# Performance work log

Hardware: AMD Instinct MI355X
Metric: run time of the kernel (lower is better)

Reference implementation:

```python
import jax, jax.numpy as jnp
import numpy as np

N, C, E = 50000, 64, 800000
EPS = 1e-5

def _ln(h, g, b):
    mu = jnp.mean(h, axis=-1, keepdims=True)
    var = jnp.var(h, axis=-1, keepdims=True)
    return (h - mu) * jax.lax.rsqrt(var + EPS) * g + b

def setup_inputs() -> dict:
    key = jax.random.key(0)
    ks = jax.random.split(key, 16)
    def w(k, i, o):
        return jax.random.normal(k, (i, o), jnp.float32) * (1.0 / np.sqrt(i))
    return {
        "x": jax.random.normal(ks[0], (N, C), jnp.float32),
        "edge_index": jax.random.randint(ks[1], (2, E), 0, N, jnp.int32),
        # structure_predictor: Linear(2C,256) -> LN(256) -> GELU -> Dropout(eval) -> Linear(256,1)
        "sp_w1": w(ks[2], 2 * C, 256), "sp_b1": jnp.zeros((256,), jnp.float32),
        "sp_g": jnp.ones((256,), jnp.float32), "sp_be": jnp.zeros((256,), jnp.float32),
        "sp_w2": w(ks[3], 256, 1), "sp_b2": jnp.zeros((1,), jnp.float32),
        # feature_reconstructor: Linear(C,2C) -> LN(2C) -> GELU -> Dropout(eval) -> Linear(2C,C)
        "fr_w1": w(ks[4], C, 2 * C), "fr_b1": jnp.zeros((2 * C,), jnp.float32),
        "fr_g": jnp.ones((2 * C,), jnp.float32), "fr_be": jnp.zeros((2 * C,), jnp.float32),
        "fr_w2": w(ks[5], 2 * C, C), "fr_b2": jnp.zeros((C,), jnp.float32),
        # projection_head: Linear(C,256) -> LN(256) -> GELU -> Linear(256,128)
        "ph_w1": w(ks[6], C, 256), "ph_b1": jnp.zeros((256,), jnp.float32),
        "ph_g": jnp.ones((256,), jnp.float32), "ph_be": jnp.zeros((256,), jnp.float32),
        "ph_w2": w(ks[7], 256, 128), "ph_b2": jnp.zeros((128,), jnp.float32),
    }

def reference(x, edge_index, sp_w1, sp_b1, sp_g, sp_be, sp_w2, sp_b2,
              fr_w1, fr_b1, fr_g, fr_be, fr_w2, fr_b2,
              ph_w1, ph_b1, ph_g, ph_be, ph_w2, ph_b2):
    row, col = edge_index[0], edge_index[1]
    edge_features = jnp.concatenate([x[row], x[col]], axis=1)  # [E, 2C]
    h = _ln(edge_features @ sp_w1 + sp_b1, sp_g, sp_be)
    structure_pred = jax.nn.gelu(h, approximate=False) @ sp_w2 + sp_b2  # [E, 1]
    h = _ln(x @ fr_w1 + fr_b1, fr_g, fr_be)
    reconstructed = jax.nn.gelu(h, approximate=False) @ fr_w2 + fr_b2  # [N, C]
    h = _ln(x @ ph_w1 + ph_b1, ph_g, ph_be)
    projected = jax.nn.gelu(h, approximate=False) @ ph_w2 + ph_b2  # [N, 128]
    return (structure_pred, reconstructed, projected)
```

## Files before the change

### kernel.cpp

```cpp
#include <hip/hip_runtime.h>
#include <hip/hip_bf16.h>

typedef __attribute__((ext_vector_type(8))) short short8;
typedef __attribute__((ext_vector_type(4))) float f32x4;

#define MFMA(a, b, c) __builtin_amdgcn_mfma_f32_16x16x32_bf16((a), (b), (c), 0, 0, 0)

__device__ __forceinline__ unsigned short f2bf(float f) {
    unsigned int u = __float_as_uint(f);
    u += 0x7fffu + ((u >> 16) & 1u);
    return (unsigned short)(u >> 16);
}

__device__ __forceinline__ unsigned int cvt_pk_bf16(float lo, float hi) {
    unsigned int d;
    asm("v_cvt_pk_bf16_f32 %0, %1, %2" : "=v"(d) : "v"(lo), "v"(hi));
    return d;
}

template<int CTRL>
__device__ __forceinline__ float dpp_addf(float v) {
    int t = __builtin_amdgcn_update_dpp(0, __float_as_int(v), CTRL, 0xF, 0xF, true);
    return v + __int_as_float(t);
}
__device__ __forceinline__ float rowsum16(float v) {
    v = dpp_addf<0x121>(v);
    v = dpp_addf<0x122>(v);
    v = dpp_addf<0x124>(v);
    v = dpp_addf<0x128>(v);
    return v;
}

#if __has_builtin(__builtin_amdgcn_exp2f)
#define EXP2(x) __builtin_amdgcn_exp2f(x)
#else
#define EXP2(x) __expf((x) * 0.69314718f)
#endif

__device__ __forceinline__ float gelu_fast(float x) {
    float a = x * __builtin_fmaf(x * x, 0.10295427f, 2.3021210f);
    float E = EXP2(a);
    float r = __builtin_amdgcn_rcpf(E + 1.0f);
    return __builtin_fmaf(-x, r, x);
}

__device__ __forceinline__ short8 load_bfrag(const float* __restrict__ w, int k0, int n, int ldn) {
    short8 r;
#pragma unroll
    for (int u = 0; u < 8; ++u)
        r[u] = (short)f2bf(w[(k0 + u) * ldn + n]);
    return r;
}

template<int N1P>
struct SmemMlp {
    unsigned short sS[64 * N1P];
    float rstat[64 * 8];
};

template<int K, int N1, int N2, int MI>
__device__ void mlp_tile(SmemMlp<N1 + 8>& sm, const float* __restrict__ x,
                         const float* __restrict__ w1, const float* __restrict__ b1,
                         const float* __restrict__ g, const float* __restrict__ be,
                         const float* __restrict__ w2, const float* __restrict__ b2,
                         float* __restrict__ out, int Nrows, int t) {
    constexpr int R = MI * 16;
    constexpr int KP = K + 8, N1P = N1 + 8;
    constexpr int CPW1 = N1 / 4;
    constexpr int JT1 = CPW1 / 16;
    constexpr int KK1 = K / 32;
    constexpr int KK2 = N1 / 32;
    constexpr int JT2 = N2 / 64;
    constexpr int TPR = 256 / R;
    constexpr int FPT = K / TPR;
    constexpr int F4 = FPT / 4;

    const int tid = threadIdx.x;
    const int wave = tid >> 6, lane = tid & 63;
    const int l15 = lane & 15, quad = lane >> 4;
    const int r0 = t * R;

    {
        int m0 = tid / TPR, pp = tid % TPR;
        int rowg = r0 + m0; if (rowg >= Nrows) rowg = Nrows - 1;
        const float4* src = (const float4*)(x + (long)rowg * K + pp * FPT);
        unsigned short* dst = &sm.sS[m0 * KP + pp * FPT];
#pragma unroll
        for (int u = 0; u < F4; ++u) {
            float4 f = src[u];
            ushort4 h; h.x = f2bf(f.x); h.y = f2bf(f.y); h.z = f2bf(f.z); h.w = f2bf(f.w);
            *(ushort4*)(dst + 4 * u) = h;
        }
    }

    short8 breg1[JT1][KK1];
#pragma unroll
    for (int j = 0; j < JT1; ++j)
#pragma unroll
        for (int kk = 0; kk < KK1; ++kk)
            breg1[j][kk] = load_bfrag(w1, kk * 32 + quad * 8, CPW1 * wave + 16 * j + l15, N1);

    float b1v[JT1], gv[JT1], bev[JT1];
#pragma unroll
    for (int j = 0; j < JT1; ++j) {
        int c = CPW1 * wave + 16 * j + l15;
        b1v[j] = b1[c]; gv[j] = g[c]; bev[j] = be[c];
    }
    float b2v[JT2];
#pragma unroll
    for (int j = 0; j < JT2; ++j) b2v[j] = b2[wave * 16 * JT2 + 16 * j + l15];

    __syncthreads();

    f32x4 acc1[MI][JT1];
#pragma unroll
    for (int i = 0; i < MI; ++i)
#pragma unroll
        for (int j = 0; j < JT1; ++j)
            acc1[i][j] = (f32x4){0.f, 0.f, 0.f, 0.f};

#pragma unroll
    for (int kk = 0; kk < KK1; ++kk) {
        short8 a[MI];
#pragma unroll
        for (int i = 0; i < MI; ++i)
            a[i] = *(const short8*)&sm.sS[(16 * i + l15) * KP + kk * 32 + quad * 8];
#pragma unroll
        for (int i = 0; i < MI; ++i)
#pragma unroll
            for (int j = 0; j < JT1; ++j)
                acc1[i][j] = MFMA(a[i], breg1[j][kk], acc1[i][j]);
    }

#pragma unroll
    for (int i = 0; i < MI; ++i)
#pragma unroll
        for (int r = 0; r < 4; ++r) {
            float s = 0.f, ss = 0.f;
#pragma unroll
            for (int j = 0; j < JT1; ++j) {
                float v = acc1[i][j][r] + b1v[j];
                acc1[i][j][r] = v;
                s += v; ss = __builtin_fmaf(v, v, ss);
            }
            s = rowsum16(s); ss = rowsum16(ss);
            if (l15 == 0) {
                int row = 16 * i + quad * 4 + r;
                *(float2*)&sm.rstat[row * 8 + wave * 2] = make_float2(s, ss);
            }
        }
    __syncthreads();

#pragma unroll
    for (int i = 0; i < MI; ++i)
#pragma unroll
        for (int r = 0; r < 4; ++r) {
            int row = 16 * i + quad * 4 + r;
            const float4* st = (const float4*)&sm.rstat[row * 8];
            float4 q0 = st[0], q1 = st[1];
            float s  = (q0.x + q0.z) + (q1.x + q1.z);
            float ss = (q0.y + q0.w) + (q1.y + q1.w);
            float mean = s * (1.f / (float)N1);
            float var  = __builtin_fmaf(ss, 1.f / (float)N1, -mean * mean);
            float rstd = __builtin_amdgcn_rsqf(var + 1e-5f);
            float nm = -mean * rstd;
#pragma unroll
            for (int j = 0; j < JT1; ++j) {
                float tt = __builtin_fmaf(acc1[i][j][r], rstd, nm);
                float xn = __builtin_fmaf(tt, gv[j], bev[j]);
                sm.sS[row * N1P + CPW1 * wave + 16 * j + l15] = f2bf(gelu_fast(xn));
            }
        }
    __syncthreads();

    f32x4 acc2[MI][JT2];
#pragma unroll
    for (int i = 0; i < MI; ++i)
#pragma unroll
        for (int j = 0; j < JT2; ++j)
            acc2[i][j] = (f32x4){0.f, 0.f, 0.f, 0.f};

#pragma unroll
    for (int kk = 0; kk < KK2; ++kk) {
        short8 bf[JT2];
#pragma unroll
        for (int j = 0; j < JT2; ++j)
            bf[j] = load_bfrag(w2, kk * 32 + quad * 8, wave * 16 * JT2 + 16 * j + l15, N2);
        short8 a[MI];
#pragma unroll
        for (int i = 0; i < MI; ++i)
            a[i] = *(const short8*)&sm.sS[(16 * i + l15) * N1P + kk * 32 + quad * 8];
#pragma unroll
        for (int i = 0; i < MI; ++i)
#pragma unroll
            for (int j = 0; j < JT2; ++j)
                acc2[i][j] = MFMA(a[i], bf[j], acc2[i][j]);
    }

#pragma unroll
    for (int i = 0; i < MI; ++i)
#pragma unroll
        for (int r = 0; r < 4; ++r) {
            int rowg = r0 + 16 * i + quad * 4 + r;
            if (rowg < Nrows) {
#pragma unroll
                for (int j = 0; j < JT2; ++j)
                    out[(long)rowg * N2 + wave * 16 * JT2 + 16 * j + l15] = acc2[i][j][r] + b2v[j];
            }
        }
}

__device__ void proj_tile(unsigned short* sX , const float* __restrict__ x,
                          const float* __restrict__ w1, const float* __restrict__ b1,
                          unsigned short* __restrict__ P, int N, int tile, int isB) {
    constexpr int KP = 72;
    const int tid = threadIdx.x;
    const int wave = tid >> 6, lane = tid & 63;
    const int l15 = lane & 15, quad = lane >> 4;
    const int r0 = tile * 64;

    {
        int m0 = tid >> 2, pp = tid & 3;
        int rowg = r0 + m0; if (rowg >= N) rowg = N - 1;
        const float4* src = (const float4*)(x + (long)rowg * 64 + pp * 16);
        unsigned short* dst = &sX[m0 * KP + pp * 16];
#pragma unroll
        for (int u = 0; u < 4; ++u) {
            float4 f = src[u];
            ushort4 h; h.x = f2bf(f.x); h.y = f2bf(f.y); h.z = f2bf(f.z); h.w = f2bf(f.w);
            *(ushort4*)(dst + 4 * u) = h;
        }
    }

    short8 breg[4][2];
#pragma unroll
    for (int j = 0; j < 4; ++j)
#pragma unroll
        for (int kk = 0; kk < 2; ++kk)
            breg[j][kk] = load_bfrag(w1, isB * 64 + kk * 32 + quad * 8, wave * 64 + 16 * j + l15, 256);

    float b1v[4];
#pragma unroll
    for (int j = 0; j < 4; ++j)
        b1v[j] = isB ? 0.f : b1[wave * 64 + 16 * j + l15];

    __syncthreads();

    f32x4 acc[4][4];
#pragma unroll
    for (int i = 0; i < 4; ++i)
#pragma unroll
        for (int j = 0; j < 4; ++j)
            acc[i][j] = (f32x4){0.f, 0.f, 0.f, 0.f};

#pragma unroll
    for (int kk = 0; kk < 2; ++kk) {
        short8 a[4];
#pragma unroll
        for (int i = 0; i < 4; ++i)
            a[i] = *(const short8*)&sX[(16 * i + l15) * KP + kk * 32 + quad * 8];
#pragma unroll
        for (int i = 0; i < 4; ++i)
#pragma unroll
            for (int j = 0; j < 4; ++j)
                acc[i][j] = MFMA(a[i], breg[j][kk], acc[i][j]);
    }

#pragma unroll
    for (int i = 0; i < 4; ++i)
#pragma unroll
        for (int r = 0; r < 4; ++r) {
            int rowg = r0 + 16 * i + quad * 4 + r;
            if (rowg < N) {
                uint2 d;
                d.x = cvt_pk_bf16(acc[i][0][r] + b1v[0], acc[i][1][r] + b1v[1]);
                d.y = cvt_pk_bf16(acc[i][2][r] + b1v[2], acc[i][3][r] + b1v[3]);
                *(uint2*)(P + (long)rowg * 256 + wave * 64 + l15 * 4) = d;
            }
        }
}

__device__ __forceinline__ int clamp_e(long v, int E) {
    return v < (long)E ? (int)v : E - 1;
}

__device__ void edge_role2(const unsigned short* __restrict__ Pa,
                           const unsigned short* __restrict__ Pb,
                           const int* __restrict__ ei,
                           const float* __restrict__ g, const float* __restrict__ be,
                           const float* __restrict__ w2, const float* __restrict__ b2,
                           float* __restrict__ out, int E, int ebid, int nebk) {
    const int tid = threadIdx.x;
    const int lane = tid & 63;
    const int quad = lane >> 4, l15 = lane & 15;

    float gv[16], bev[16], w2v[16];
#pragma unroll
    for (int u = 0; u < 16; ++u) {
        int c = ((l15 >> 2) << 6) + ((u & 3) << 4) + ((l15 & 3) << 2) + (u >> 2);
        gv[u] = g[c]; bev[u] = be[c]; w2v[u] = w2[c];
    }
    const float b2v = b2[0];

    const int wid = ebid * 4 + (tid >> 6);
    const long stride = (long)nebk * 16L;
    long base = (long)wid * 4;
    if (base >= E) return;

    int ir1, ic1;
    uint4 cA0, cA1, cB0, cB1;
    {
        int e0 = clamp_e(base + quad, E);
        int r = ei[e0], c = ei[E + e0];
        const uint4* pa = (const uint4*)(Pa + (long)r * 256 + l15 * 16);
        const uint4* pb = (const uint4*)(Pb + (long)c * 256 + l15 * 16);
        cA0 = pa[0]; cA1 = pa[1]; cB0 = pb[0]; cB1 = pb[1];
        int e1 = clamp_e(base + stride + quad, E);
        ir1 = ei[e1]; ic1 = ei[E + e1];
    }

    for (; base < E; base += stride) {
        int e2 = clamp_e(base + 2 * stride + quad, E);
        int ir2 = ei[e2];
        int ic2 = ei[E + e2];
        const uint4* pa = (const uint4*)(Pa + (long)ir1 * 256 + l15 * 16);
        const uint4* pb = (const uint4*)(Pb + (long)ic1 * 256 + l15 * 16);
        uint4 nA0 = pa[0], nA1 = pa[1], nB0 = pb[0], nB1 = pb[1];

        unsigned int av[8] = {cA0.x, cA0.y, cA0.z, cA0.w, cA1.x, cA1.y, cA1.z, cA1.w};
        unsigned int bv[8] = {cB0.x, cB0.y, cB0.z, cB0.w, cB1.x, cB1.y, cB1.z, cB1.w};

        float h[16];
#pragma unroll
        for (int k = 0; k < 8; ++k) {
            float alo = __uint_as_float(av[k] << 16);
            float ahi = __uint_as_float(av[k] & 0xffff0000u);
            float blo = __uint_as_float(bv[k] << 16);
            float bhi = __uint_as_float(bv[k] & 0xffff0000u);
            h[2*k]   = alo + blo;
            h[2*k+1] = ahi + bhi;
        }

        float s = 0.f, ss = 0.f;
#pragma unroll
        for (int u = 0; u < 16; ++u) {
            s += h[u];
            ss = __builtin_fmaf(h[u], h[u], ss);
        }
        s = rowsum16(s); ss = rowsum16(ss);

        float mean = s * (1.f / 256.f);
        float var  = __builtin_fmaf(ss, 1.f / 256.f, -mean * mean);
        float rstd = __builtin_amdgcn_rsqf(var + 1e-5f);
        float nm = -mean * rstd;

        float spp = 0.f;
#pragma unroll
        for (int u = 0; u < 16; ++u) {
            float tt = __builtin_fmaf(h[u], rstd, nm);
            float xn = __builtin_fmaf(tt, gv[u], bev[u]);
            spp = __builtin_fmaf(gelu_fast(xn), w2v[u], spp);
        }
        spp = rowsum16(spp);
        long eL = base + quad;
        if (l15 == 0 && eL < E) out[eL] = spp + b2v;

        cA0 = nA0; cA1 = nA1; cB0 = nB0; cB1 = nB1;
        ir1 = ir2; ic1 = ic2;
    }
}

__global__ __launch_bounds__(256, 3)
void proj_kernel(const float* __restrict__ x, const float* __restrict__ w1,
                 const float* __restrict__ b1, unsigned short* __restrict__ Pa,
                 unsigned short* __restrict__ Pb, int N, int ntN) {
    __shared__ unsigned short sX[64 * 72];
    const int q = blockIdx.x;
    const int isB = q >= ntN;
    const int tile = isB ? q - ntN : q;
    proj_tile(sX, x, w1, b1, isB ? Pb : Pa, N, tile, isB);
}

union SmemHeads {
    SmemMlp<136> a;
    SmemMlp<264> b;
};

__global__ __launch_bounds__(256, 3)
void heads_kernel(const float* __restrict__ x,
                  const float* __restrict__ fr_w1, const float* __restrict__ fr_b1,
                  const float* __restrict__ fr_g, const float* __restrict__ fr_be,
                  const float* __restrict__ fr_w2, const float* __restrict__ fr_b2,
                  const float* __restrict__ ph_w1, const float* __restrict__ ph_b1,
                  const float* __restrict__ ph_g, const float* __restrict__ ph_be,
                  const float* __restrict__ ph_w2, const float* __restrict__ ph_b2,
                  float* __restrict__ out_rec, float* __restrict__ out_proj,
                  int N, int nFR) {
    __shared__ SmemHeads sm;
    const int b = blockIdx.x;
    if (b < nFR)
        mlp_tile<64, 128, 64, 4>(sm.a, x, fr_w1, fr_b1, fr_g, fr_be, fr_w2, fr_b2,
                                 out_rec, N, b);
    else
        mlp_tile<64, 256, 128, 2>(sm.b, x, ph_w1, ph_b1, ph_g, ph_be, ph_w2, ph_b2,
                                  out_proj, N, b - nFR);
}

__global__ __launch_bounds__(256)
void edge_stream(const unsigned short* __restrict__ Pa, const unsigned short* __restrict__ Pb,
                 const int* __restrict__ ei,
                 const float* __restrict__ g, const float* __restrict__ be,
                 const float* __restrict__ w2, const float* __restrict__ b2,
                 float* __restrict__ out, int E) {
    edge_role2(Pa, Pb, ei, g, be, w2, b2, out, E, blockIdx.x, gridDim.x);
}

struct SmemEdge {
    unsigned short sA[2][32 * 136];
    float rstat[32 * 8];
    float spL[32 * 4];
};
union SmemU {
    SmemEdge e;
    SmemMlp<136> a;
    SmemMlp<264> b;
};

__device__ void edge_role(SmemEdge& sm, const float* __restrict__ x, const int* __restrict__ ei,
                          const float* __restrict__ w1, const float* __restrict__ b1,
                          const float* __restrict__ g, const float* __restrict__ be,
                          const float* __restrict__ w2, const float* __restrict__ b2,
                          float* __restrict__ out, int E, int bid, int nblocks) {
    constexpr int KP = 136;
    const int tid = threadIdx.x;
    const int cw = tid >> 6, lane = tid & 63;
    const int l15 = lane & 15, quad = lane >> 4;

    short8 breg[4][4];
#pragma unroll
    for (int j = 0; j < 4; ++j)
#pragma unroll
        for (int kk = 0; kk < 4; ++kk)
            breg[j][kk] = load_bfrag(w1, kk * 32 + quad * 8, cw * 64 + 16 * j + l15, 256);

    float b1v[4], gv[4], bev[4], w2v[4];
#pragma unroll
    for (int j = 0; j < 4; ++j) {
        int c = cw * 64 + 16 * j + l15;
        b1v[j] = b1[c]; gv[j] = g[c]; bev[j] = be[c]; w2v[j] = w2[c];
    }
    const float b2v = b2[0];

    const int ntiles = (E + 31) >> 5;
    const int eLoc = tid >> 3, p = tid & 7;
    const int node = p >> 2, foff = (p & 3) * 16;

    float4 pf[4];
    auto issue = [&](int t) {
        int e = t * 32 + eLoc; if (e >= E) e = E - 1;
        int idx = ei[node * E + e];
        const float4* src = (const float4*)(x + (long)idx * 64 + foff);
#pragma unroll
        for (int u = 0; u < 4; ++u) pf[u] = src[u];
    };
    auto stage = [&](int buf) {
        unsigned short* dst = &sm.sA[buf][eLoc * KP + node * 64 + foff];
#pragma unroll
        for (int u = 0; u < 4; ++u) {
            ushort4 h;
            h.x = f2bf(pf[u].x); h.y = f2bf(pf[u].y);
            h.z = f2bf(pf[u].z); h.w = f2bf(pf[u].w);
            *(ushort4*)(dst + 4 * u) = h;
        }
    };

    int t = bid;
    if (t >= ntiles) return;
    issue(t); stage(0);
    if (t + nblocks < ntiles) issue(t + nblocks);
    __syncthreads();
    int cur = 0;

    for (; t < ntiles; t += nblocks) {
        f32x4 acc[2][4];
#pragma unroll
        for (int i = 0; i < 2; ++i)
#pragma unroll
            for (int j = 0; j < 4; ++j)
                acc[i][j] = (f32x4){0.f, 0.f, 0.f, 0.f};

#pragma unroll
        for (int kk = 0; kk < 4; ++kk) {
            short8 a[2];
#pragma unroll
            for (int i = 0; i < 2; ++i)
                a[i] = *(const short8*)&sm.sA[cur][(16 * i + l15) * KP + kk * 32 + quad * 8];
#pragma unroll
            for (int i = 0; i < 2; ++i)
#pragma unroll
                for (int j = 0; j < 4; ++j)
                    acc[i][j] = MFMA(a[i], breg[j][kk], acc[i][j]);
        }

        if (t + nblocks < ntiles) {
            stage(cur ^ 1);
            if (t + 2 * nblocks < ntiles) issue(t + 2 * nblocks);
        }

#pragma unroll
        for (int i = 0; i < 2; ++i)
#pragma unroll
            for (int r = 0; r < 4; ++r) {
                float v0 = acc[i][0][r] + b1v[0];
                float v1 = acc[i][1][r] + b1v[1];
                float v2 = acc[i][2][r] + b1v[2];
                float v3 = acc[i][3][r] + b1v[3];
                acc[i][0][r] = v0; acc[i][1][r] = v1; acc[i][2][r] = v2; acc[i][3][r] = v3;
                float s  = (v0 + v1) + (v2 + v3);
                float ss = __builtin_fmaf(v0, v0, __builtin_fmaf(v1, v1,
                           __builtin_fmaf(v2, v2, v3 * v3)));
                s = rowsum16(s); ss = rowsum16(ss);
                if (l15 == 0) {
                    int row = 16 * i + quad * 4 + r;
                    *(float2*)&sm.rstat[row * 8 + cw * 2] = make_float2(s, ss);
                }
            }
        __syncthreads();

#pragma unroll
        for (int i = 0; i < 2; ++i)
#pragma unroll
            for (int r = 0; r < 4; ++r) {
                int row = 16 * i + quad * 4 + r;
                const float4* st = (const float4*)&sm.rstat[row * 8];
                float4 q0 = st[0], q1 = st[1];
                float s  = (q0.x + q0.z) + (q1.x + q1.z);
                float ss = (q0.y + q0.w) + (q1.y + q1.w);
                float mean = s * (1.f / 256.f);
                float var  = __builtin_fmaf(ss, 1.f / 256.f, -mean * mean);
                float rstd = __builtin_amdgcn_rsqf(var + 1e-5f);
                float nm = -mean * rstd;
                float spp = 0.f;
#pragma unroll
                for (int j = 0; j < 4; ++j) {
                    float tt = __builtin_fmaf(acc[i][j][r], rstd, nm);
                    float xn = __builtin_fmaf(tt, gv[j], bev[j]);
                    spp = __builtin_fmaf(gelu_fast(xn), w2v[j], spp);
                }
                spp = rowsum16(spp);
                if (l15 == 0) sm.spL[row * 4 + cw] = spp;
            }
        __syncthreads();

        if (tid < 32) {
            int e = t * 32 + tid;
            if (e < E) {
                const float4* sp = (const float4*)&sm.spL[tid * 4];
                float4 u0 = sp[0];
                out[e] = ((u0.x + u0.y) + (u0.z + u0.w)) + b2v;
            }
        }
        cur ^= 1;
    }
}

__global__ __launch_bounds__(256, 3)
void fused_all(const float* __restrict__ x, const int* __restrict__ ei,
               const float* __restrict__ sp_w1, const float* __restrict__ sp_b1,
               const float* __restrict__ sp_g, const float* __restrict__ sp_be,
               const float* __restrict__ sp_w2, const float* __restrict__ sp_b2,
               const float* __restrict__ fr_w1, const float* __restrict__ fr_b1,
               const float* __restrict__ fr_g, const float* __restrict__ fr_be,
               const float* __restrict__ fr_w2, const float* __restrict__ fr_b2,
               const float* __restrict__ ph_w1, const float* __restrict__ ph_b1,
               const float* __restrict__ ph_g, const float* __restrict__ ph_be,
               const float* __restrict__ ph_w2, const float* __restrict__ ph_b2,
               float* __restrict__ out_sp, float* __restrict__ out_rec,
               float* __restrict__ out_proj, int N, int E) {
    __shared__ SmemU sm;
    const int b = blockIdx.x;
    if (b < 128) {
        for (int tt = b; tt < (N + 63) / 64; tt += 128)
            mlp_tile<64, 128, 64, 4>(sm.a, x, fr_w1, fr_b1, fr_g, fr_be, fr_w2, fr_b2,
                                     out_rec, N, tt);
    } else if (b < 256) {
        for (int tt = b - 128; tt < (N + 31) / 32; tt += 128)
            mlp_tile<64, 256, 128, 2>(sm.b, x, ph_w1, ph_b1, ph_g, ph_be, ph_w2, ph_b2,
                                      out_proj, N, tt);
    } else {
        edge_role(sm.e, x, ei, sp_w1, sp_b1, sp_g, sp_be, sp_w2, sp_b2,
                  out_sp, E, b - 256, 1024);
    }
}

extern "C" void kernel_launch(void* const* d_in, const int* in_sizes, int n_in,
                              void* d_out, int out_size, void* d_ws, size_t ws_size,
                              hipStream_t stream) {
    const float* x     = (const float*)d_in[0];
    const int*   ei    = (const int*)d_in[1];
    const float* sp_w1 = (const float*)d_in[2];
    const float* sp_b1 = (const float*)d_in[3];
    const float* sp_g  = (const float*)d_in[4];
    const float* sp_be = (const float*)d_in[5];
    const float* sp_w2 = (const float*)d_in[6];
    const float* sp_b2 = (const float*)d_in[7];
    const float* fr_w1 = (const float*)d_in[8];
    const float* fr_b1 = (const float*)d_in[9];
    const float* fr_g  = (const float*)d_in[10];
    const float* fr_be = (const float*)d_in[11];
    const float* fr_w2 = (const float*)d_in[12];
    const float* fr_b2 = (const float*)d_in[13];
    const float* ph_w1 = (const float*)d_in[14];
    const float* ph_b1 = (const float*)d_in[15];
    const float* ph_g  = (const float*)d_in[16];
    const float* ph_be = (const float*)d_in[17];
    const float* ph_w2 = (const float*)d_in[18];
    const float* ph_b2 = (const float*)d_in[19];

    const int N = in_sizes[0] / 64;
    const int E = in_sizes[1] / 2;

    float* out_sp   = (float*)d_out;
    float* out_rec  = out_sp + E;
    float* out_proj = out_rec + (size_t)N * 64;

    const size_t needed = 2ull * (size_t)N * 256 * sizeof(unsigned short);
    if (ws_size >= needed) {
        unsigned short* Pa = (unsigned short*)d_ws;
        unsigned short* Pb = Pa + (size_t)N * 256;
        const int ntN = (N + 63) / 64;
        const int nFR = (N + 63) / 64;
        const int nPH = (N + 31) / 32;

        proj_kernel<<<dim3(2 * ntN), dim3(256), 0, stream>>>(
            x, sp_w1, sp_b1, Pa, Pb, N, ntN);

        heads_kernel<<<dim3(nFR + nPH), dim3(256), 0, stream>>>(
            x, fr_w1, fr_b1, fr_g, fr_be, fr_w2, fr_b2,
            ph_w1, ph_b1, ph_g, ph_be, ph_w2, ph_b2,
            out_rec, out_proj, N, nFR);

        edge_stream<<<dim3(2048), dim3(256), 0, stream>>>(
            Pa, Pb, ei, sp_g, sp_be, sp_w2, sp_b2, out_sp, E);
    } else {
        fused_all<<<dim3(1280), dim3(256), 0, stream>>>(
            x, ei, sp_w1, sp_b1, sp_g, sp_be, sp_w2, sp_b2,
            fr_w1, fr_b1, fr_g, fr_be, fr_w2, fr_b2,
            ph_w1, ph_b1, ph_g, ph_be, ph_w2, ph_b2,
            out_sp, out_rec, out_proj, N, E);
    }
}
```

Baseline: 273.8 us.

## Merge projection and head kernels into one launch; pack edge math as float2

Combines the edge-projection kernel and the two MLP-head kernels into a single prep kernel whose blocks are dispatched by index, with the heavier projection-head tiles first. This removes one launch and lets the three kinds of work fill the GPU together. The edge streaming loop is rewritten with two-wide float vectors so the compiler can emit packed FP32 instructions for the unpack, LayerNorm and GELU arithmetic. The fallback fused kernel also gains a barrier between looped tiles, which fixes reuse of shared memory across iterations.

```diff
diff --git a/kernel.cpp b/kernel.cpp
--- a/kernel.cpp
+++ b/kernel.cpp
@@ -3,6 +3,7 @@
 
 typedef __attribute__((ext_vector_type(8))) short short8;
 typedef __attribute__((ext_vector_type(4))) float f32x4;
+typedef __attribute__((ext_vector_type(2))) float f32x2;
 
 #define MFMA(a, b, c) __builtin_amdgcn_mfma_f32_16x16x32_bf16((a), (b), (c), 0, 0, 0)
 
@@ -42,6 +43,24 @@
     float E = EXP2(a);
     float r = __builtin_amdgcn_rcpf(E + 1.0f);
     return __builtin_fmaf(-x, r, x);
+}
+
+__device__ __forceinline__ f32x2 gelu_fast2(f32x2 x) {
+    f32x2 c1 = {2.3021210f, 2.3021210f}, c2 = {0.10295427f, 0.10295427f};
+    f32x2 a = x * __builtin_elementwise_fma(x * x, c2, c1);
+    f32x2 E;
+    E[0] = EXP2(a[0]); E[1] = EXP2(a[1]);
+    f32x2 Ep = E + (f32x2){1.f, 1.f};
+    f32x2 r;
+    r[0] = __builtin_amdgcn_rcpf(Ep[0]); r[1] = __builtin_amdgcn_rcpf(Ep[1]);
+    return __builtin_elementwise_fma(-x, r, x);
+}
+
+__device__ __forceinline__ f32x2 unpk_bf2(unsigned int a) {
+    f32x2 r;
+    r[0] = __uint_as_float(a << 16);
+    r[1] = __uint_as_float(a & 0xffff0000u);
+    return r;
 }
 
 __device__ __forceinline__ short8 load_bfrag(const float* __restrict__ w, int k0, int n, int ldn) {
@@ -294,11 +313,15 @@
     const int lane = tid & 63;
     const int quad = lane >> 4, l15 = lane & 15;
 
-    float gv[16], bev[16], w2v[16];
-#pragma unroll
-    for (int u = 0; u < 16; ++u) {
-        int c = ((l15 >> 2) << 6) + ((u & 3) << 4) + ((l15 & 3) << 2) + (u >> 2);
-        gv[u] = g[c]; bev[u] = be[c]; w2v[u] = w2[c];
+    f32x2 gv2[8], bev2[8], w2v2[8];
+#pragma unroll
+    for (int k = 0; k < 8; ++k) {
+#pragma unroll
+        for (int h = 0; h < 2; ++h) {
+            int u = 2 * k + h;
+            int c = ((l15 >> 2) << 6) + ((u & 3) << 4) + ((l15 & 3) << 2) + (u >> 2);
+            gv2[k][h] = g[c]; bev2[k][h] = be[c]; w2v2[k][h] = w2[c];
+        }
     }
     const float b2v = b2[0];
 
@@ -330,38 +353,31 @@
         unsigned int av[8] = {cA0.x, cA0.y, cA0.z, cA0.w, cA1.x, cA1.y, cA1.z, cA1.w};
         unsigned int bv[8] = {cB0.x, cB0.y, cB0.z, cB0.w, cB1.x, cB1.y, cB1.z, cB1.w};
 
-        float h[16];
+        f32x2 h2[8];
+        f32x2 s2 = {0.f, 0.f}, ss2 = {0.f, 0.f};
 #pragma unroll
         for (int k = 0; k < 8; ++k) {
-            float alo = __uint_as_float(av[k] << 16);
-            float ahi = __uint_as_float(av[k] & 0xffff0000u);
-            float blo = __uint_as_float(bv[k] << 16);
-            float bhi = __uint_as_float(bv[k] & 0xffff0000u);
-            h[2*k]   = alo + blo;
-            h[2*k+1] = ahi + bhi;
-        }
-
-        float s = 0.f, ss = 0.f;
-#pragma unroll
-        for (int u = 0; u < 16; ++u) {
-            s += h[u];
-            ss = __builtin_fmaf(h[u], h[u], ss);
-        }
+            h2[k] = unpk_bf2(av[k]) + unpk_bf2(bv[k]);
+            s2 = s2 + h2[k];
+            ss2 = __builtin_elementwise_fma(h2[k], h2[k], ss2);
+        }
+        float s = s2[0] + s2[1], ss = ss2[0] + ss2[1];
         s = rowsum16(s); ss = rowsum16(ss);
 
         float mean = s * (1.f / 256.f);
         float var  = __builtin_fmaf(ss, 1.f / 256.f, -mean * mean);
         float rstd = __builtin_amdgcn_rsqf(var + 1e-5f);
         float nm = -mean * rstd;
-
-        float spp = 0.f;
-#pragma unroll
-        for (int u = 0; u < 16; ++u) {
-            float tt = __builtin_fmaf(h[u], rstd, nm);
-            float xn = __builtin_fmaf(tt, gv[u], bev[u]);
-            spp = __builtin_fmaf(gelu_fast(xn), w2v[u], spp);
-        }
-        spp = rowsum16(spp);
+        f32x2 rstd2 = {rstd, rstd}, nm2 = {nm, nm};
+
+        f32x2 spp2 = {0.f, 0.f};
+#pragma unroll
+        for (int k = 0; k < 8; ++k) {
+            f32x2 tt = __builtin_elementwise_fma(h2[k], rstd2, nm2);
+            f32x2 xn = __builtin_elementwise_fma(tt, gv2[k], bev2[k]);
+            spp2 = __builtin_elementwise_fma(gelu_fast2(xn), w2v2[k], spp2);
+        }
+        float spp = rowsum16(spp2[0] + spp2[1]);
         long eL = base + quad;
         if (l15 == 0 && eL < E) out[eL] = spp + b2v;
 
@@ -370,40 +386,38 @@
     }
 }
 
-__global__ __launch_bounds__(256, 3)
-void proj_kernel(const float* __restrict__ x, const float* __restrict__ w1,
-                 const float* __restrict__ b1, unsigned short* __restrict__ Pa,
-                 unsigned short* __restrict__ Pb, int N, int ntN) {
-    __shared__ unsigned short sX[64 * 72];
-    const int q = blockIdx.x;
-    const int isB = q >= ntN;
-    const int tile = isB ? q - ntN : q;
-    proj_tile(sX, x, w1, b1, isB ? Pb : Pa, N, tile, isB);
-}
-
-union SmemHeads {
+union SmemPrep {
+    unsigned short sX[64 * 72];
     SmemMlp<136> a;
     SmemMlp<264> b;
 };
 
 __global__ __launch_bounds__(256, 3)
-void heads_kernel(const float* __restrict__ x,
-                  const float* __restrict__ fr_w1, const float* __restrict__ fr_b1,
-                  const float* __restrict__ fr_g, const float* __restrict__ fr_be,
-                  const float* __restrict__ fr_w2, const float* __restrict__ fr_b2,
-                  const float* __restrict__ ph_w1, const float* __restrict__ ph_b1,
-                  const float* __restrict__ ph_g, const float* __restrict__ ph_be,
-                  const float* __restrict__ ph_w2, const float* __restrict__ ph_b2,
-                  float* __restrict__ out_rec, float* __restrict__ out_proj,
-                  int N, int nFR) {
-    __shared__ SmemHeads sm;
+void prep_kernel(const float* __restrict__ x,
+                 const float* __restrict__ sp_w1, const float* __restrict__ sp_b1,
+                 const float* __restrict__ fr_w1, const float* __restrict__ fr_b1,
+                 const float* __restrict__ fr_g, const float* __restrict__ fr_be,
+                 const float* __restrict__ fr_w2, const float* __restrict__ fr_b2,
+                 const float* __restrict__ ph_w1, const float* __restrict__ ph_b1,
+                 const float* __restrict__ ph_g, const float* __restrict__ ph_be,
+                 const float* __restrict__ ph_w2, const float* __restrict__ ph_b2,
+                 unsigned short* __restrict__ Pa, unsigned short* __restrict__ Pb,
+                 float* __restrict__ out_rec, float* __restrict__ out_proj,
+                 int N, int ntN, int nFR, int nPH) {
+    __shared__ SmemPrep sm;
     const int b = blockIdx.x;
-    if (b < nFR)
+    if (b < nPH) {
+        mlp_tile<64, 256, 128, 2>(sm.b, x, ph_w1, ph_b1, ph_g, ph_be, ph_w2, ph_b2,
+                                  out_proj, N, b);
+    } else if (b < nPH + nFR) {
         mlp_tile<64, 128, 64, 4>(sm.a, x, fr_w1, fr_b1, fr_g, fr_be, fr_w2, fr_b2,
-                                 out_rec, N, b);
-    else
-        mlp_tile<64, 256, 128, 2>(sm.b, x, ph_w1, ph_b1, ph_g, ph_be, ph_w2, ph_b2,
-                                  out_proj, N, b - nFR);
+                                 out_rec, N, b - nPH);
+    } else {
+        int q = b - nPH - nFR;
+        int isB = q >= ntN;
+        int tile = isB ? q - ntN : q;
+        proj_tile(sm.sX, x, sp_w1, sp_b1, isB ? Pb : Pa, N, tile, isB);
+    }
 }
 
 __global__ __launch_bounds__(256)
@@ -580,13 +594,17 @@
     __shared__ SmemU sm;
     const int b = blockIdx.x;
     if (b < 128) {
-        for (int tt = b; tt < (N + 63) / 64; tt += 128)
+        for (int tt = b; tt < (N + 63) / 64; tt += 128) {
+            __syncthreads();
             mlp_tile<64, 128, 64, 4>(sm.a, x, fr_w1, fr_b1, fr_g, fr_be, fr_w2, fr_b2,
                                      out_rec, N, tt);
+        }
     } else if (b < 256) {
-        for (int tt = b - 128; tt < (N + 31) / 32; tt += 128)
+        for (int tt = b - 128; tt < (N + 31) / 32; tt += 128) {
+            __syncthreads();
             mlp_tile<64, 256, 128, 2>(sm.b, x, ph_w1, ph_b1, ph_g, ph_be, ph_w2, ph_b2,
                                       out_proj, N, tt);
+        }
     } else {
         edge_role(sm.e, x, ei, sp_w1, sp_b1, sp_g, sp_be, sp_w2, sp_b2,
                   out_sp, E, b - 256, 1024);
@@ -632,13 +650,11 @@
         const int nFR = (N + 63) / 64;
         const int nPH = (N + 31) / 32;
 
-        proj_kernel<<<dim3(2 * ntN), dim3(256), 0, stream>>>(
-            x, sp_w1, sp_b1, Pa, Pb, N, ntN);
-
-        heads_kernel<<<dim3(nFR + nPH), dim3(256), 0, stream>>>(
-            x, fr_w1, fr_b1, fr_g, fr_be, fr_w2, fr_b2,
+        prep_kernel<<<dim3(nPH + nFR + 2 * ntN), dim3(256), 0, stream>>>(
+            x, sp_w1, sp_b1,
+            fr_w1, fr_b1, fr_g, fr_be, fr_w2, fr_b2,
             ph_w1, ph_b1, ph_g, ph_be, ph_w2, ph_b2,
-            out_rec, out_proj, N, nFR);
+            Pa, Pb, out_rec, out_proj, N, ntN, nFR, nPH);
 
         edge_stream<<<dim3(2048), dim3(256), 0, stream>>>(
             Pa, Pb, ei, sp_g, sp_be, sp_w2, sp_b2, out_sp, E);
```

Measured after the change: 259.8 us. 5.1% less time.
